# Optimization experiments

Measured on AMD Instinct MI355X. Metric: run time of the kernel, lower is better.

## Reference

```python
import jax, jax.numpy as jnp
import numpy as np

N_NODES = 100000
N_EDGES = 640000
D_IN = 128
D_H = 128


def setup_inputs() -> dict:
    key = jax.random.key(0)
    ks = jax.random.split(key, 24)
    def W(k, shp):
        return jax.random.normal(k, shp, dtype=jnp.float32) * 0.05
    inp = {
        "x": jax.random.normal(ks[0], (N_NODES, D_IN), dtype=jnp.float32),
        "src": jax.random.randint(ks[1], (N_EDGES,), 0, N_NODES, dtype=jnp.int32),
        "dst": jax.random.randint(ks[2], (N_EDGES,), 0, N_NODES, dtype=jnp.int32),
        "neg_src": jax.random.randint(ks[3], (N_EDGES,), 0, N_NODES, dtype=jnp.int32),
        "neg_dst": jax.random.randint(ks[4], (N_EDGES,), 0, N_NODES, dtype=jnp.int32),
        # SAGEConv layer 1/2/3: fc_self weight, fc_neigh weight (stored [in,out]), bias
        "Ws1": W(ks[5], (D_IN, D_H)), "Wn1": W(ks[6], (D_IN, D_H)), "b1": jnp.zeros((D_H,), jnp.float32),
        "Ws2": W(ks[7], (D_H, D_H)), "Wn2": W(ks[8], (D_H, D_H)), "b2": jnp.zeros((D_H,), jnp.float32),
        "Ws3": W(ks[9], (D_H, D_H)), "Wn3": W(ks[10], (D_H, D_H)), "b3": jnp.zeros((D_H,), jnp.float32),
        # MLPPredictor: W1 [2h,h], W2 [h,1]
        "Wp1": W(ks[11], (2 * D_H, D_H)), "bp1": jnp.zeros((D_H,), jnp.float32),
        "Wp2": W(ks[12], (D_H, 1)), "bp2": jnp.zeros((1,), jnp.float32),
    }
    return inp


def _sage_mean(x, src, dst, Ws, Wn, b):
    # DGL SAGEConv 'mean': rst = fc_self(h) + fc_neigh(mean_{in-neighbors}(h)) + bias
    n = x.shape[0]
    msum = jax.ops.segment_sum(x[src], dst, num_segments=n)        # [N, d]
    deg = jax.ops.segment_sum(jnp.ones_like(src, dtype=x.dtype), dst, num_segments=n)
    mean = msum / jnp.clip(deg, 1.0)[:, None]                      # zero for isolated nodes
    return x @ Ws + mean @ Wn + b


def _edge_score(h, s, d, Wp1, bp1, Wp2, bp2):
    z = jnp.concatenate([h[s], h[d]], axis=1)                      # [E, 2h]
    return (jax.nn.relu(z @ Wp1 + bp1) @ Wp2 + bp2)[:, 0]          # [E]


def reference(x, src, dst, neg_src, neg_dst,
              Ws1, Wn1, b1, Ws2, Wn2, b2, Ws3, Wn3, b3,
              Wp1, bp1, Wp2, bp2):
    h = _sage_mean(x, src, dst, Ws1, Wn1, b1)
    h = _sage_mean(h, src, dst, Ws2, Wn2, b2)
    h = _sage_mean(h, src, dst, Ws3, Wn3, b3)
    pos = _edge_score(h, src, dst, Wp1, bp1, Wp2, bp2)
    neg = _edge_score(h, neg_src, neg_dst, Wp1, bp1, Wp2, bp2)
    return (pos, neg)
```

## Files before the change

### kernel.cpp

```cpp
#include <hip/hip_runtime.h>

#define N_NODES 100000
#define N_EDGES 640000
#define D 128
#define SCAN_TILE 1024
#define SCAN_BLOCKS ((N_NODES + SCAN_TILE - 1) / SCAN_TILE)

typedef __attribute__((ext_vector_type(8))) short bf16x8;
typedef __attribute__((ext_vector_type(4))) float f32x4;

__device__ __forceinline__ unsigned short f32_to_bf16(float f) {
  union { float f; unsigned int u; } v; v.f = f;
  unsigned int u = v.u;
  unsigned int r = (u + 0x7fffu + ((u >> 16) & 1u)) >> 16;
  return (unsigned short)r;
}
__device__ __forceinline__ float bf16_lo(unsigned int u) { return __uint_as_float(u << 16); }
__device__ __forceinline__ float bf16_hi(unsigned int u) { return __uint_as_float(u & 0xffff0000u); }

__global__ void zero_i32(int* __restrict__ p, int n) {
  int i = blockIdx.x * blockDim.x + threadIdx.x;
  if (i < n) p[i] = 0;
}

__global__ void f32_to_bf16_vec(const float* __restrict__ in, unsigned short* __restrict__ out, int n4) {
  int i = blockIdx.x * blockDim.x + threadIdx.x;
  if (i < n4) {
    float4 v = ((const float4*)in)[i];
    ushort4 o;
    o.x = f32_to_bf16(v.x); o.y = f32_to_bf16(v.y);
    o.z = f32_to_bf16(v.z); o.w = f32_to_bf16(v.w);
    ((ushort4*)out)[i] = o;
  }
}

__global__ void transpose_w(const float* __restrict__ W0, const float* __restrict__ W1,
                            const float* __restrict__ W2, const float* __restrict__ W3,
                            const float* __restrict__ W4, const float* __restrict__ W5,
                            const float* __restrict__ W6, const float* __restrict__ W7,
                            unsigned short* __restrict__ wt) {
  int id = blockIdx.x * 256 + threadIdx.x;
  int mat = id >> 14;
  int rem = id & 16383;
  int n = rem >> 7, k = rem & 127;
  const float* Wm = mat < 4 ? (mat < 2 ? (mat == 0 ? W0 : W1) : (mat == 2 ? W2 : W3))
                            : (mat < 6 ? (mat == 4 ? W4 : W5) : (mat == 6 ? W6 : W7));
  wt[id] = f32_to_bf16(Wm[k * D + n]);
}

__global__ void hist_kernel(const int* __restrict__ dst, int* __restrict__ deg, int E) {
  int i = blockIdx.x * blockDim.x + threadIdx.x;
  if (i < E) atomicAdd(&deg[dst[i]], 1);
}

__global__ void scan_blocksum(const int* __restrict__ deg, int* __restrict__ partial, int n) {
  __shared__ int lds[256];
  const int tid = threadIdx.x;
  const int base = blockIdx.x * SCAN_TILE + tid * 4;
  int s = 0;
#pragma unroll
  for (int j = 0; j < 4; ++j) {
    int i = base + j;
    if (i < n) s += deg[i];
  }
  lds[tid] = s;
  __syncthreads();
  for (int off = 128; off > 0; off >>= 1) {
    if (tid < off) lds[tid] += lds[tid + off];
    __syncthreads();
  }
  if (tid == 0) partial[blockIdx.x] = lds[0];
}

__global__ void scan_offsets(int* __restrict__ partial, int* __restrict__ row_start, int nb, int n) {
  __shared__ int lds[128];
  const int tid = threadIdx.x;
  int v = (tid < nb) ? partial[tid] : 0;
  lds[tid] = v;
  __syncthreads();
  for (int off = 1; off < 128; off <<= 1) {
    int t = (tid >= off) ? lds[tid - off] : 0;
    __syncthreads();
    lds[tid] += t;
    __syncthreads();
  }
  if (tid < nb) partial[tid] = (tid == 0) ? 0 : lds[tid - 1];
  if (tid == 0) row_start[n] = lds[nb - 1];
}

__global__ void scan_final(const int* __restrict__ deg, const int* __restrict__ partial,
                           int* __restrict__ row_start, int n) {
  __shared__ int lds[256];
  const int tid = threadIdx.x;
  const int base = blockIdx.x * SCAN_TILE + tid * 4;
  int d[4];
  int s = 0;
#pragma unroll
  for (int j = 0; j < 4; ++j) {
    int i = base + j;
    d[j] = (i < n) ? deg[i] : 0;
    s += d[j];
  }
  lds[tid] = s;
  __syncthreads();
  for (int off = 1; off < 256; off <<= 1) {
    int t = (tid >= off) ? lds[tid - off] : 0;
    __syncthreads();
    lds[tid] += t;
    __syncthreads();
  }
  int pre = partial[blockIdx.x] + lds[tid] - s;
#pragma unroll
  for (int j = 0; j < 4; ++j) {
    int i = base + j;
    if (i < n) {
      row_start[i] = pre;
      pre += d[j];
    }
  }
}

__global__ void fill_kernel(const int* __restrict__ src, const int* __restrict__ dst,
                            const int* __restrict__ row_start, int* __restrict__ cursor,
                            int* __restrict__ esrc, int E) {
  int i = blockIdx.x * blockDim.x + threadIdx.x;
  if (i < E) {
    int d = dst[i];
    int pos = atomicAdd(&cursor[d], 1);
    esrc[row_start[d] + pos] = src[i];
  }
}

__global__ void aggregate_wave(const unsigned short* __restrict__ h, const int* __restrict__ row_start,
                               const int* __restrict__ esrc, unsigned short* __restrict__ mean, int n) {
  const int node = (blockIdx.x * blockDim.x + threadIdx.x) >> 6;
  const int lane = threadIdx.x & 63;
  if (node >= n) return;
  const int q = lane >> 4;
  const int fl = lane & 15;
  const int s0 = row_start[node], s1 = row_start[node + 1];
  float acc[8] = {0.f, 0.f, 0.f, 0.f, 0.f, 0.f, 0.f, 0.f};
  for (int e = s0 + q; e < s1; e += 4) {
    int s = esrc[e];
    uint4 raw = *(const uint4*)(h + (size_t)s * D + fl * 8);
    acc[0] += bf16_lo(raw.x); acc[1] += bf16_hi(raw.x);
    acc[2] += bf16_lo(raw.y); acc[3] += bf16_hi(raw.y);
    acc[4] += bf16_lo(raw.z); acc[5] += bf16_hi(raw.z);
    acc[6] += bf16_lo(raw.w); acc[7] += bf16_hi(raw.w);
  }
#pragma unroll
  for (int j = 0; j < 8; ++j) {
    acc[j] += __shfl_xor(acc[j], 16);
    acc[j] += __shfl_xor(acc[j], 32);
  }
  if (q == 0) {
    const float inv = 1.0f / (float)max(s1 - s0, 1);
    uint4 o;
    o.x = (unsigned)f32_to_bf16(acc[0] * inv) | ((unsigned)f32_to_bf16(acc[1] * inv) << 16);
    o.y = (unsigned)f32_to_bf16(acc[2] * inv) | ((unsigned)f32_to_bf16(acc[3] * inv) << 16);
    o.z = (unsigned)f32_to_bf16(acc[4] * inv) | ((unsigned)f32_to_bf16(acc[5] * inv) << 16);
    o.w = (unsigned)f32_to_bf16(acc[6] * inv) | ((unsigned)f32_to_bf16(acc[7] * inv) << 16);
    *(uint4*)(mean + (size_t)node * D + fl * 8) = o;
  }
}

template <int NCHUNK, bool FP32OUT>
__global__ __launch_bounds__(256) void gemm_mfma(
    const unsigned short* __restrict__ in0, const unsigned short* __restrict__ in1,
    const unsigned short* __restrict__ Wt0, const unsigned short* __restrict__ Wt1,
    const float* __restrict__ bias, void* __restrict__ out, int M) {
  __shared__ unsigned short wl[128][136];
  const int tid = threadIdx.x;
  const int lane = tid & 63;
  const int wave = tid >> 6;
  const int m0 = blockIdx.x * 64 + wave * 16;
  const int row = lane & 15;
  const int q = lane >> 4;
  const int mload = min(m0 + row, M - 1);

  bf16x8 afrag[NCHUNK * 4];
#pragma unroll
  for (int s = 0; s < NCHUNK * 4; ++s) {
    const unsigned short* srcp = (NCHUNK == 2 && s >= 4) ? in1 : in0;
    afrag[s] = *reinterpret_cast<const bf16x8*>(srcp + (size_t)mload * D + (s & 3) * 32 + q * 8);
  }
  f32x4 acc[8];
#pragma unroll
  for (int t = 0; t < 8; ++t) acc[t] = (f32x4){0.f, 0.f, 0.f, 0.f};

  for (int c = 0; c < NCHUNK; ++c) {
    const unsigned short* wsrc = (c == 0) ? Wt0 : Wt1;
    if (c) __syncthreads();
#pragma unroll
    for (int i = 0; i < 8; ++i) {
      int seg = i * 256 + tid;
      int r = seg >> 4;
      int o = (seg & 15) * 8;
      *reinterpret_cast<bf16x8*>(&wl[r][o]) =
          *reinterpret_cast<const bf16x8*>(wsrc + r * D + o);
    }
    __syncthreads();
#pragma unroll
    for (int s = 0; s < 4; ++s) {
#pragma unroll
      for (int t = 0; t < 8; ++t) {
        const int n = t * 16 + row;
        bf16x8 b = *reinterpret_cast<const bf16x8*>(&wl[n][s * 32 + q * 8]);
        acc[t] = __builtin_amdgcn_mfma_f32_16x16x32_bf16(afrag[c * 4 + s], b, acc[t], 0, 0, 0);
      }
    }
  }

#pragma unroll
  for (int t = 0; t < 8; ++t) {
    const int col = t * 16 + row;
    const float bv = bias ? bias[col] : 0.f;
#pragma unroll
    for (int r = 0; r < 4; ++r) {
      int m = m0 + q * 4 + r;
      if (m < M) {
        float v = acc[t][r] + bv;
        if (FP32OUT)
          ((float*)out)[(size_t)m * D + col] = v;
        else
          ((unsigned short*)out)[(size_t)m * D + col] = f32_to_bf16(v);
      }
    }
  }
}

__global__ __launch_bounds__(256) void gemm_pred(
    const unsigned short* __restrict__ in,
    const unsigned short* __restrict__ WtA, const unsigned short* __restrict__ WtB,
    const float* __restrict__ biasA,
    unsigned short* __restrict__ outA, unsigned short* __restrict__ outB, int M) {
  __shared__ unsigned short wl[128][136];
  const int tid = threadIdx.x;
  const int lane = tid & 63;
  const int wave = tid >> 6;
  const int m0 = blockIdx.x * 64 + wave * 16;
  const int row = lane & 15;
  const int q = lane >> 4;
  const int mload = min(m0 + row, M - 1);

  bf16x8 afrag[4];
#pragma unroll
  for (int s = 0; s < 4; ++s)
    afrag[s] = *reinterpret_cast<const bf16x8*>(in + (size_t)mload * D + s * 32 + q * 8);

  f32x4 acc[8];
  for (int pass = 0; pass < 2; ++pass) {
    const unsigned short* wsrc = pass ? WtB : WtA;
    if (pass) __syncthreads();
#pragma unroll
    for (int i = 0; i < 8; ++i) {
      int seg = i * 256 + tid;
      int r = seg >> 4;
      int o = (seg & 15) * 8;
      *reinterpret_cast<bf16x8*>(&wl[r][o]) =
          *reinterpret_cast<const bf16x8*>(wsrc + r * D + o);
    }
    __syncthreads();
#pragma unroll
    for (int t = 0; t < 8; ++t) acc[t] = (f32x4){0.f, 0.f, 0.f, 0.f};
#pragma unroll
    for (int s = 0; s < 4; ++s) {
#pragma unroll
      for (int t = 0; t < 8; ++t) {
        const int n = t * 16 + row;
        bf16x8 b = *reinterpret_cast<const bf16x8*>(&wl[n][s * 32 + q * 8]);
        acc[t] = __builtin_amdgcn_mfma_f32_16x16x32_bf16(afrag[s], b, acc[t], 0, 0, 0);
      }
    }
    unsigned short* outp = pass ? outB : outA;
#pragma unroll
    for (int t = 0; t < 8; ++t) {
      const int col = t * 16 + row;
      const float bv = pass ? 0.f : biasA[col];
#pragma unroll
      for (int r = 0; r < 4; ++r) {
        int m = m0 + q * 4 + r;
        if (m < M) outp[(size_t)m * D + col] = f32_to_bf16(acc[t][r] + bv);
      }
    }
    if (pass == 0) __syncthreads();
  }
}

__global__ void edge_score_fused(const unsigned short* __restrict__ A, const unsigned short* __restrict__ B,
                                 const int* __restrict__ ps, const int* __restrict__ pd,
                                 const int* __restrict__ ns, const int* __restrict__ nd,
                                 const float* __restrict__ Wp2, const float* __restrict__ bp2,
                                 float* __restrict__ out, int E) {
  const int t = blockIdx.x * blockDim.x + threadIdx.x;
  const int e = t >> 4;
  const int fl = threadIdx.x & 15;
  if (e >= E) return;
  const int si = ps[e], di = pd[e];
  const int nsi = ns[e], ndi = nd[e];
  uint4 ra = *(const uint4*)(A + (size_t)si * D + fl * 8);
  uint4 rb = *(const uint4*)(B + (size_t)di * D + fl * 8);
  uint4 rna = *(const uint4*)(A + (size_t)nsi * D + fl * 8);
  uint4 rnb = *(const uint4*)(B + (size_t)ndi * D + fl * 8);
  float4 w0 = *(const float4*)(Wp2 + fl * 8);
  float4 w1 = *(const float4*)(Wp2 + fl * 8 + 4);

  float pp =
      fmaxf(bf16_lo(ra.x) + bf16_lo(rb.x), 0.f) * w0.x +
      fmaxf(bf16_hi(ra.x) + bf16_hi(rb.x), 0.f) * w0.y +
      fmaxf(bf16_lo(ra.y) + bf16_lo(rb.y), 0.f) * w0.z +
      fmaxf(bf16_hi(ra.y) + bf16_hi(rb.y), 0.f) * w0.w +
      fmaxf(bf16_lo(ra.z) + bf16_lo(rb.z), 0.f) * w1.x +
      fmaxf(bf16_hi(ra.z) + bf16_hi(rb.z), 0.f) * w1.y +
      fmaxf(bf16_lo(ra.w) + bf16_lo(rb.w), 0.f) * w1.z +
      fmaxf(bf16_hi(ra.w) + bf16_hi(rb.w), 0.f) * w1.w;
  float pn =
      fmaxf(bf16_lo(rna.x) + bf16_lo(rnb.x), 0.f) * w0.x +
      fmaxf(bf16_hi(rna.x) + bf16_hi(rnb.x), 0.f) * w0.y +
      fmaxf(bf16_lo(rna.y) + bf16_lo(rnb.y), 0.f) * w0.z +
      fmaxf(bf16_hi(rna.y) + bf16_hi(rnb.y), 0.f) * w0.w +
      fmaxf(bf16_lo(rna.z) + bf16_lo(rnb.z), 0.f) * w1.x +
      fmaxf(bf16_hi(rna.z) + bf16_hi(rnb.z), 0.f) * w1.y +
      fmaxf(bf16_lo(rna.w) + bf16_lo(rnb.w), 0.f) * w1.z +
      fmaxf(bf16_hi(rna.w) + bf16_hi(rnb.w), 0.f) * w1.w;

  pp += __shfl_xor(pp, 1);  pn += __shfl_xor(pn, 1);
  pp += __shfl_xor(pp, 2);  pn += __shfl_xor(pn, 2);
  pp += __shfl_xor(pp, 4);  pn += __shfl_xor(pn, 4);
  pp += __shfl_xor(pp, 8);  pn += __shfl_xor(pn, 8);
  if (fl == 0) {
    float b = bp2[0];
    out[e] = pp + b;
    out[E + e] = pn + b;
  }
}

extern "C" void kernel_launch(void* const* d_in, const int* in_sizes, int n_in,
                              void* d_out, int out_size, void* d_ws, size_t ws_size,
                              hipStream_t stream) {
  const float* x = (const float*)d_in[0];
  const int* src = (const int*)d_in[1];
  const int* dst = (const int*)d_in[2];
  const int* nsrc = (const int*)d_in[3];
  const int* ndst = (const int*)d_in[4];
  const float* Ws1 = (const float*)d_in[5];
  const float* Wn1 = (const float*)d_in[6];
  const float* b1 = (const float*)d_in[7];
  const float* Ws2 = (const float*)d_in[8];
  const float* Wn2 = (const float*)d_in[9];
  const float* b2 = (const float*)d_in[10];
  const float* Ws3 = (const float*)d_in[11];
  const float* Wn3 = (const float*)d_in[12];
  const float* b3 = (const float*)d_in[13];
  const float* Wp1 = (const float*)d_in[14];
  const float* bp1 = (const float*)d_in[15];
  const float* Wp2 = (const float*)d_in[16];
  const float* bp2 = (const float*)d_in[17];
  float* out = (float*)d_out;

  char* ws = (char*)d_ws;
  size_t off = 0;
  auto alloc = [&](size_t bytes) -> void* {
    void* p = ws + off;
    off += (bytes + 255) & ~(size_t)255;
    return p;
  };
  const size_t NODE_F32 = sizeof(float) * (size_t)N_NODES * D;
  char* region0 = (char*)alloc(NODE_F32);
  char* region1 = (char*)alloc(NODE_F32);
  int* row_start = (int*)alloc(sizeof(int) * (N_NODES + 1));
  int* deg = (int*)alloc(sizeof(int) * N_NODES * 2);
  int* cursor = deg + N_NODES;
  int* esrc = (int*)alloc(sizeof(int) * N_EDGES);
  int* partial = (int*)alloc(sizeof(int) * 128);
  unsigned short* wt = (unsigned short*)alloc(sizeof(unsigned short) * 8 * D * D);
  (void)ws_size;

  unsigned short* xb = (unsigned short*)region0;
  unsigned short* meanb = xb + (size_t)N_NODES * D;
  unsigned short* hA = (unsigned short*)region1;
  unsigned short* hB = hA + (size_t)N_NODES * D;
  unsigned short* Ab = xb;
  unsigned short* Bb = meanb;

  f32_to_bf16_vec<<<(N_NODES * D / 4 + 255) / 256, 256, 0, stream>>>(x, xb, N_NODES * D / 4);
  transpose_w<<<512, 256, 0, stream>>>(Ws1, Wn1, Ws2, Wn2, Ws3, Wn3, Wp1, Wp1 + D * D, wt);

  zero_i32<<<(2 * N_NODES + 255) / 256, 256, 0, stream>>>(deg, 2 * N_NODES);
  hist_kernel<<<(N_EDGES + 255) / 256, 256, 0, stream>>>(dst, deg, N_EDGES);
  scan_blocksum<<<SCAN_BLOCKS, 256, 0, stream>>>(deg, partial, N_NODES);
  scan_offsets<<<1, 128, 0, stream>>>(partial, row_start, SCAN_BLOCKS, N_NODES);
  scan_final<<<SCAN_BLOCKS, 256, 0, stream>>>(deg, partial, row_start, N_NODES);
  fill_kernel<<<(N_EDGES + 255) / 256, 256, 0, stream>>>(src, dst, row_start, cursor, esrc, N_EDGES);

  const int aggBlocks = (N_NODES * 64 + 255) / 256;
  const int gemmBlocks = (N_NODES + 63) / 64;
  const int edgeBlocks = (N_EDGES * 16) / 256;

  aggregate_wave<<<aggBlocks, 256, 0, stream>>>(xb, row_start, esrc, meanb, N_NODES);
  gemm_mfma<2, false><<<gemmBlocks, 256, 0, stream>>>(xb, meanb, wt, wt + 16384, b1, hA, N_NODES);
  aggregate_wave<<<aggBlocks, 256, 0, stream>>>(hA, row_start, esrc, meanb, N_NODES);
  gemm_mfma<2, false><<<gemmBlocks, 256, 0, stream>>>(hA, meanb, wt + 2 * 16384, wt + 3 * 16384, b2, hB, N_NODES);
  aggregate_wave<<<aggBlocks, 256, 0, stream>>>(hB, row_start, esrc, meanb, N_NODES);
  gemm_mfma<2, false><<<gemmBlocks, 256, 0, stream>>>(hB, meanb, wt + 4 * 16384, wt + 5 * 16384, b3, hA, N_NODES);
  gemm_pred<<<gemmBlocks, 256, 0, stream>>>(hA, wt + 6 * 16384, wt + 7 * 16384, bp1, Ab, Bb, N_NODES);
  edge_score_fused<<<edgeBlocks, 256, 0, stream>>>(Ab, Bb, src, dst, nsrc, ndst, Wp2, bp2, out, N_EDGES);
}
```

Before: 514.1 us.

## Fuse neighbor mean aggregation with SAGE GEMM and predictor projection per tile

Each layer now uses one kernel that gathers the neighbor mean for a 64-node tile into shared memory and feeds it straight into the MFMA GEMM. This avoids writing the mean buffer to global memory and reading it back. The last layer also computes both predictor projections in the same kernel, which removes separate launches. The cost is lower gather parallelism: 16 lanes now handle one node at a time, processing 4 nodes in sequence with 4-way unrolled edge loads, where before a full wave handled each node. Extra shared memory may also reduce occupancy.

```diff
diff --git a/kernel.cpp b/kernel.cpp
--- a/kernel.cpp
+++ b/kernel.cpp
@@ -17,6 +17,13 @@
 }
 __device__ __forceinline__ float bf16_lo(unsigned int u) { return __uint_as_float(u << 16); }
 __device__ __forceinline__ float bf16_hi(unsigned int u) { return __uint_as_float(u & 0xffff0000u); }
+
+__device__ __forceinline__ void acc8(float* a, uint4 r) {
+  a[0] += bf16_lo(r.x); a[1] += bf16_hi(r.x);
+  a[2] += bf16_lo(r.y); a[3] += bf16_hi(r.y);
+  a[4] += bf16_lo(r.z); a[5] += bf16_hi(r.z);
+  a[6] += bf16_lo(r.w); a[7] += bf16_hi(r.w);
+}
 
 __global__ void zero_i32(int* __restrict__ p, int n) {
   int i = blockIdx.x * blockDim.x + threadIdx.x;
@@ -131,159 +138,184 @@
   }
 }
 
-__global__ void aggregate_wave(const unsigned short* __restrict__ h, const int* __restrict__ row_start,
-                               const int* __restrict__ esrc, unsigned short* __restrict__ mean, int n) {
-  const int node = (blockIdx.x * blockDim.x + threadIdx.x) >> 6;
-  const int lane = threadIdx.x & 63;
-  if (node >= n) return;
-  const int q = lane >> 4;
-  const int fl = lane & 15;
-  const int s0 = row_start[node], s1 = row_start[node + 1];
-  float acc[8] = {0.f, 0.f, 0.f, 0.f, 0.f, 0.f, 0.f, 0.f};
-  for (int e = s0 + q; e < s1; e += 4) {
-    int s = esrc[e];
-    uint4 raw = *(const uint4*)(h + (size_t)s * D + fl * 8);
-    acc[0] += bf16_lo(raw.x); acc[1] += bf16_hi(raw.x);
-    acc[2] += bf16_lo(raw.y); acc[3] += bf16_hi(raw.y);
-    acc[4] += bf16_lo(raw.z); acc[5] += bf16_hi(raw.z);
-    acc[6] += bf16_lo(raw.w); acc[7] += bf16_hi(raw.w);
-  }
-#pragma unroll
-  for (int j = 0; j < 8; ++j) {
-    acc[j] += __shfl_xor(acc[j], 16);
-    acc[j] += __shfl_xor(acc[j], 32);
-  }
-  if (q == 0) {
-    const float inv = 1.0f / (float)max(s1 - s0, 1);
-    uint4 o;
-    o.x = (unsigned)f32_to_bf16(acc[0] * inv) | ((unsigned)f32_to_bf16(acc[1] * inv) << 16);
-    o.y = (unsigned)f32_to_bf16(acc[2] * inv) | ((unsigned)f32_to_bf16(acc[3] * inv) << 16);
-    o.z = (unsigned)f32_to_bf16(acc[4] * inv) | ((unsigned)f32_to_bf16(acc[5] * inv) << 16);
-    o.w = (unsigned)f32_to_bf16(acc[6] * inv) | ((unsigned)f32_to_bf16(acc[7] * inv) << 16);
-    *(uint4*)(mean + (size_t)node * D + fl * 8) = o;
-  }
-}
-
-template <int NCHUNK, bool FP32OUT>
-__global__ __launch_bounds__(256) void gemm_mfma(
-    const unsigned short* __restrict__ in0, const unsigned short* __restrict__ in1,
-    const unsigned short* __restrict__ Wt0, const unsigned short* __restrict__ Wt1,
-    const float* __restrict__ bias, void* __restrict__ out, int M) {
+template <bool PRED>
+__global__ __launch_bounds__(256) void layer_fused(
+    const unsigned short* __restrict__ hin,
+    const int* __restrict__ row_start, const int* __restrict__ esrc,
+    const unsigned short* __restrict__ Wts, const unsigned short* __restrict__ Wtn,
+    const float* __restrict__ bias,
+    const unsigned short* __restrict__ WtA, const unsigned short* __restrict__ WtB,
+    const float* __restrict__ biasA,
+    unsigned short* __restrict__ out0, unsigned short* __restrict__ out1, int M) {
   __shared__ unsigned short wl[128][136];
+  __shared__ unsigned short mt[64][136];
   const int tid = threadIdx.x;
   const int lane = tid & 63;
   const int wave = tid >> 6;
-  const int m0 = blockIdx.x * 64 + wave * 16;
+  const int m0 = blockIdx.x * 64;
   const int row = lane & 15;
   const int q = lane >> 4;
-  const int mload = min(m0 + row, M - 1);
-
-  bf16x8 afrag[NCHUNK * 4];
-#pragma unroll
-  for (int s = 0; s < NCHUNK * 4; ++s) {
-    const unsigned short* srcp = (NCHUNK == 2 && s >= 4) ? in1 : in0;
-    afrag[s] = *reinterpret_cast<const bf16x8*>(srcp + (size_t)mload * D + (s & 3) * 32 + q * 8);
-  }
+  const int mw = m0 + wave * 16;
+  const int mload = min(mw + row, M - 1);
+
+#pragma unroll
+  for (int i = 0; i < 8; ++i) {
+    int seg = i * 256 + tid;
+    int r = seg >> 4, o = (seg & 15) * 8;
+    *reinterpret_cast<bf16x8*>(&wl[r][o]) = *reinterpret_cast<const bf16x8*>(Wts + r * D + o);
+  }
+  bf16x8 ah[4];
+#pragma unroll
+  for (int s = 0; s < 4; ++s)
+    ah[s] = *reinterpret_cast<const bf16x8*>(hin + (size_t)mload * D + s * 32 + q * 8);
+
+  {
+    const int g = tid >> 4;
+    const int fl = tid & 15;
+    for (int j = 0; j < 4; ++j) {
+      const int node = m0 + g * 4 + j;
+      float ac[8] = {0.f, 0.f, 0.f, 0.f, 0.f, 0.f, 0.f, 0.f};
+      if (node < M) {
+        const int s0 = row_start[node], s1 = row_start[node + 1];
+        int e = s0;
+        for (; e + 4 <= s1; e += 4) {
+          int i0 = esrc[e], i1 = esrc[e + 1], i2 = esrc[e + 2], i3 = esrc[e + 3];
+          uint4 r0 = *(const uint4*)(hin + (size_t)i0 * D + fl * 8);
+          uint4 r1 = *(const uint4*)(hin + (size_t)i1 * D + fl * 8);
+          uint4 r2 = *(const uint4*)(hin + (size_t)i2 * D + fl * 8);
+          uint4 r3 = *(const uint4*)(hin + (size_t)i3 * D + fl * 8);
+          acc8(ac, r0); acc8(ac, r1); acc8(ac, r2); acc8(ac, r3);
+        }
+        for (; e < s1; ++e) {
+          uint4 r0 = *(const uint4*)(hin + (size_t)esrc[e] * D + fl * 8);
+          acc8(ac, r0);
+        }
+        const float inv = 1.0f / (float)max(s1 - s0, 1);
+#pragma unroll
+        for (int k = 0; k < 8; ++k) ac[k] *= inv;
+      }
+      uint4 o;
+      o.x = (unsigned)f32_to_bf16(ac[0]) | ((unsigned)f32_to_bf16(ac[1]) << 16);
+      o.y = (unsigned)f32_to_bf16(ac[2]) | ((unsigned)f32_to_bf16(ac[3]) << 16);
+      o.z = (unsigned)f32_to_bf16(ac[4]) | ((unsigned)f32_to_bf16(ac[5]) << 16);
+      o.w = (unsigned)f32_to_bf16(ac[6]) | ((unsigned)f32_to_bf16(ac[7]) << 16);
+      *reinterpret_cast<uint4*>(&mt[g * 4 + j][fl * 8]) = o;
+    }
+  }
+  __syncthreads();
+
+  const int lrow = wave * 16 + row;
+  bf16x8 am[4];
+#pragma unroll
+  for (int s = 0; s < 4; ++s)
+    am[s] = *reinterpret_cast<const bf16x8*>(&mt[lrow][s * 32 + q * 8]);
+
   f32x4 acc[8];
 #pragma unroll
   for (int t = 0; t < 8; ++t) acc[t] = (f32x4){0.f, 0.f, 0.f, 0.f};
 
-  for (int c = 0; c < NCHUNK; ++c) {
-    const unsigned short* wsrc = (c == 0) ? Wt0 : Wt1;
-    if (c) __syncthreads();
-#pragma unroll
-    for (int i = 0; i < 8; ++i) {
-      int seg = i * 256 + tid;
-      int r = seg >> 4;
-      int o = (seg & 15) * 8;
-      *reinterpret_cast<bf16x8*>(&wl[r][o]) =
-          *reinterpret_cast<const bf16x8*>(wsrc + r * D + o);
-    }
-    __syncthreads();
-#pragma unroll
-    for (int s = 0; s < 4; ++s) {
-#pragma unroll
-      for (int t = 0; t < 8; ++t) {
-        const int n = t * 16 + row;
-        bf16x8 b = *reinterpret_cast<const bf16x8*>(&wl[n][s * 32 + q * 8]);
-        acc[t] = __builtin_amdgcn_mfma_f32_16x16x32_bf16(afrag[c * 4 + s], b, acc[t], 0, 0, 0);
+#pragma unroll
+  for (int s = 0; s < 4; ++s)
+#pragma unroll
+    for (int t = 0; t < 8; ++t) {
+      bf16x8 b = *reinterpret_cast<const bf16x8*>(&wl[t * 16 + row][s * 32 + q * 8]);
+      acc[t] = __builtin_amdgcn_mfma_f32_16x16x32_bf16(ah[s], b, acc[t], 0, 0, 0);
+    }
+  __syncthreads();
+#pragma unroll
+  for (int i = 0; i < 8; ++i) {
+    int seg = i * 256 + tid;
+    int r = seg >> 4, o = (seg & 15) * 8;
+    *reinterpret_cast<bf16x8*>(&wl[r][o]) = *reinterpret_cast<const bf16x8*>(Wtn + r * D + o);
+  }
+  __syncthreads();
+#pragma unroll
+  for (int s = 0; s < 4; ++s)
+#pragma unroll
+    for (int t = 0; t < 8; ++t) {
+      bf16x8 b = *reinterpret_cast<const bf16x8*>(&wl[t * 16 + row][s * 32 + q * 8]);
+      acc[t] = __builtin_amdgcn_mfma_f32_16x16x32_bf16(am[s], b, acc[t], 0, 0, 0);
+    }
+
+  if (!PRED) {
+#pragma unroll
+    for (int t = 0; t < 8; ++t) {
+      const int col = t * 16 + row;
+      const float bv = bias[col];
+#pragma unroll
+      for (int r = 0; r < 4; ++r) {
+        int m = mw + q * 4 + r;
+        if (m < M) out0[(size_t)m * D + col] = f32_to_bf16(acc[t][r] + bv);
       }
     }
-  }
-
+    return;
+  }
+
+  __syncthreads();
 #pragma unroll
   for (int t = 0; t < 8; ++t) {
     const int col = t * 16 + row;
-    const float bv = bias ? bias[col] : 0.f;
+    const float bv = bias[col];
+#pragma unroll
+    for (int r = 0; r < 4; ++r)
+      mt[wave * 16 + q * 4 + r][col] = f32_to_bf16(acc[t][r] + bv);
+  }
+#pragma unroll
+  for (int i = 0; i < 8; ++i) {
+    int seg = i * 256 + tid;
+    int r = seg >> 4, o = (seg & 15) * 8;
+    *reinterpret_cast<bf16x8*>(&wl[r][o]) = *reinterpret_cast<const bf16x8*>(WtA + r * D + o);
+  }
+  __syncthreads();
+  bf16x8 ap[4];
+#pragma unroll
+  for (int s = 0; s < 4; ++s)
+    ap[s] = *reinterpret_cast<const bf16x8*>(&mt[lrow][s * 32 + q * 8]);
+
+#pragma unroll
+  for (int t = 0; t < 8; ++t) acc[t] = (f32x4){0.f, 0.f, 0.f, 0.f};
+#pragma unroll
+  for (int s = 0; s < 4; ++s)
+#pragma unroll
+    for (int t = 0; t < 8; ++t) {
+      bf16x8 b = *reinterpret_cast<const bf16x8*>(&wl[t * 16 + row][s * 32 + q * 8]);
+      acc[t] = __builtin_amdgcn_mfma_f32_16x16x32_bf16(ap[s], b, acc[t], 0, 0, 0);
+    }
+#pragma unroll
+  for (int t = 0; t < 8; ++t) {
+    const int col = t * 16 + row;
+    const float bv = biasA[col];
 #pragma unroll
     for (int r = 0; r < 4; ++r) {
-      int m = m0 + q * 4 + r;
-      if (m < M) {
-        float v = acc[t][r] + bv;
-        if (FP32OUT)
-          ((float*)out)[(size_t)m * D + col] = v;
-        else
-          ((unsigned short*)out)[(size_t)m * D + col] = f32_to_bf16(v);
-      }
-    }
-  }
-}
-
-__global__ __launch_bounds__(256) void gemm_pred(
-    const unsigned short* __restrict__ in,
-    const unsigned short* __restrict__ WtA, const unsigned short* __restrict__ WtB,
-    const float* __restrict__ biasA,
-    unsigned short* __restrict__ outA, unsigned short* __restrict__ outB, int M) {
-  __shared__ unsigned short wl[128][136];
-  const int tid = threadIdx.x;
-  const int lane = tid & 63;
-  const int wave = tid >> 6;
-  const int m0 = blockIdx.x * 64 + wave * 16;
-  const int row = lane & 15;
-  const int q = lane >> 4;
-  const int mload = min(m0 + row, M - 1);
-
-  bf16x8 afrag[4];
-#pragma unroll
-  for (int s = 0; s < 4; ++s)
-    afrag[s] = *reinterpret_cast<const bf16x8*>(in + (size_t)mload * D + s * 32 + q * 8);
-
-  f32x4 acc[8];
-  for (int pass = 0; pass < 2; ++pass) {
-    const unsigned short* wsrc = pass ? WtB : WtA;
-    if (pass) __syncthreads();
-#pragma unroll
-    for (int i = 0; i < 8; ++i) {
-      int seg = i * 256 + tid;
-      int r = seg >> 4;
-      int o = (seg & 15) * 8;
-      *reinterpret_cast<bf16x8*>(&wl[r][o]) =
-          *reinterpret_cast<const bf16x8*>(wsrc + r * D + o);
-    }
-    __syncthreads();
-#pragma unroll
-    for (int t = 0; t < 8; ++t) acc[t] = (f32x4){0.f, 0.f, 0.f, 0.f};
-#pragma unroll
-    for (int s = 0; s < 4; ++s) {
-#pragma unroll
-      for (int t = 0; t < 8; ++t) {
-        const int n = t * 16 + row;
-        bf16x8 b = *reinterpret_cast<const bf16x8*>(&wl[n][s * 32 + q * 8]);
-        acc[t] = __builtin_amdgcn_mfma_f32_16x16x32_bf16(afrag[s], b, acc[t], 0, 0, 0);
-      }
-    }
-    unsigned short* outp = pass ? outB : outA;
+      int m = mw + q * 4 + r;
+      if (m < M) out0[(size_t)m * D + col] = f32_to_bf16(acc[t][r] + bv);
+    }
+  }
+  __syncthreads();
+#pragma unroll
+  for (int i = 0; i < 8; ++i) {
+    int seg = i * 256 + tid;
+    int r = seg >> 4, o = (seg & 15) * 8;
+    *reinterpret_cast<bf16x8*>(&wl[r][o]) = *reinterpret_cast<const bf16x8*>(WtB + r * D + o);
+  }
+  __syncthreads();
+#pragma unroll
+  for (int t = 0; t < 8; ++t) acc[t] = (f32x4){0.f, 0.f, 0.f, 0.f};
+#pragma unroll
+  for (int s = 0; s < 4; ++s)
 #pragma unroll
     for (int t = 0; t < 8; ++t) {
-      const int col = t * 16 + row;
-      const float bv = pass ? 0.f : biasA[col];
-#pragma unroll
-      for (int r = 0; r < 4; ++r) {
-        int m = m0 + q * 4 + r;
-        if (m < M) outp[(size_t)m * D + col] = f32_to_bf16(acc[t][r] + bv);
-      }
-    }
-    if (pass == 0) __syncthreads();
+      bf16x8 b = *reinterpret_cast<const bf16x8*>(&wl[t * 16 + row][s * 32 + q * 8]);
+      acc[t] = __builtin_amdgcn_mfma_f32_16x16x32_bf16(ap[s], b, acc[t], 0, 0, 0);
+    }
+#pragma unroll
+  for (int t = 0; t < 8; ++t) {
+    const int col = t * 16 + row;
+#pragma unroll
+    for (int r = 0; r < 4; ++r) {
+      int m = mw + q * 4 + r;
+      if (m < M) out1[(size_t)m * D + col] = f32_to_bf16(acc[t][r]);
+    }
   }
 }
 
@@ -377,11 +409,10 @@
   (void)ws_size;
 
   unsigned short* xb = (unsigned short*)region0;
-  unsigned short* meanb = xb + (size_t)N_NODES * D;
   unsigned short* hA = (unsigned short*)region1;
   unsigned short* hB = hA + (size_t)N_NODES * D;
   unsigned short* Ab = xb;
-  unsigned short* Bb = meanb;
+  unsigned short* Bb = xb + (size_t)N_NODES * D;
 
   f32_to_bf16_vec<<<(N_NODES * D / 4 + 255) / 256, 256, 0, stream>>>(x, xb, N_NODES * D / 4);
   transpose_w<<<512, 256, 0, stream>>>(Ws1, Wn1, Ws2, Wn2, Ws3, Wn3, Wp1, Wp1 + D * D, wt);
@@ -393,16 +424,15 @@
   scan_final<<<SCAN_BLOCKS, 256, 0, stream>>>(deg, partial, row_start, N_NODES);
   fill_kernel<<<(N_EDGES + 255) / 256, 256, 0, stream>>>(src, dst, row_start, cursor, esrc, N_EDGES);
 
-  const int aggBlocks = (N_NODES * 64 + 255) / 256;
-  const int gemmBlocks = (N_NODES + 63) / 64;
+  const int layerBlocks = (N_NODES + 63) / 64;
   const int edgeBlocks = (N_EDGES * 16) / 256;
 
-  aggregate_wave<<<aggBlocks, 256, 0, stream>>>(xb, row_start, esrc, meanb, N_NODES);
-  gemm_mfma<2, false><<<gemmBlocks, 256, 0, stream>>>(xb, meanb, wt, wt + 16384, b1, hA, N_NODES);
-  aggregate_wave<<<aggBlocks, 256, 0, stream>>>(hA, row_start, esrc, meanb, N_NODES);
-  gemm_mfma<2, false><<<gemmBlocks, 256, 0, stream>>>(hA, meanb, wt + 2 * 16384, wt + 3 * 16384, b2, hB, N_NODES);
-  aggregate_wave<<<aggBlocks, 256, 0, stream>>>(hB, row_start, esrc, meanb, N_NODES);
-  gemm_mfma<2, false><<<gemmBlocks, 256, 0, stream>>>(hB, meanb, wt + 4 * 16384, wt + 5 * 16384, b3, hA, N_NODES);
-  gemm_pred<<<gemmBlocks, 256, 0, stream>>>(hA, wt + 6 * 16384, wt + 7 * 16384, bp1, Ab, Bb, N_NODES);
+  layer_fused<false><<<layerBlocks, 256, 0, stream>>>(
+      xb, row_start, esrc, wt, wt + 16384, b1, nullptr, nullptr, nullptr, hA, nullptr, N_NODES);
+  layer_fused<false><<<layerBlocks, 256, 0, stream>>>(
+      hA, row_start, esrc, wt + 2 * 16384, wt + 3 * 16384, b2, nullptr, nullptr, nullptr, hB, nullptr, N_NODES);
+  layer_fused<true><<<layerBlocks, 256, 0, stream>>>(
+      hB, row_start, esrc, wt + 4 * 16384, wt + 5 * 16384, b3, wt + 6 * 16384, wt + 7 * 16384, bp1,
+      Ab, Bb, N_NODES);
   edge_score_fused<<<edgeBlocks, 256, 0, stream>>>(Ab, Bb, src, dst, nsrc, ndst, Wp2, bp2, out, N_EDGES);
 }
```

After: 496.7 us. -3.4%, faster.
